# Performance work log

Measured on AMD Instinct MI355X. Metric: run time of the kernel, lower is better.

## Reference

```python
import jax, jax.numpy as jnp
import numpy as np

N_NODES = 100000
N_EDGES = 1600000
IN_DIM = 64
HID = 128
N_CLASSES = 1
N_GRAPHS = 512


def _glorot(key, shape):
    fan_in, fan_out = shape[0], shape[1]
    lim = (6.0 / (fan_in + fan_out)) ** 0.5
    return jax.random.uniform(key, shape, jnp.float32, -lim, lim)


def setup_inputs() -> dict:
    key = jax.random.key(0)
    ks = jax.random.split(key, 10)
    x = jax.random.normal(ks[0], (N_NODES, IN_DIM), jnp.float32)
    edge_src = jax.random.randint(ks[1], (N_EDGES,), 0, N_NODES)
    edge_dst = jax.random.randint(ks[2], (N_EDGES,), 0, N_NODES)
    graph_ids = jnp.sort(jax.random.randint(ks[3], (N_NODES,), 0, N_GRAPHS))
    return {
        "x": x,
        "edge_src": edge_src,
        "edge_dst": edge_dst,
        "graph_ids": graph_ids,
        "W1": _glorot(ks[4], (IN_DIM, HID)),
        "b1": jnp.zeros((HID,), jnp.float32),
        "W2": _glorot(ks[5], (HID, HID)),
        "b2": jnp.zeros((HID,), jnp.float32),
        "Wc1": _glorot(ks[6], (HID, HID)),
        "bc1": jnp.zeros((HID,), jnp.float32),
        "Wc2": _glorot(ks[7], (HID, HID)),
        "bc2": jnp.zeros((HID,), jnp.float32),
        "Wc3": _glorot(ks[8], (HID, N_CLASSES)),
        "bc3": jnp.zeros((N_CLASSES,), jnp.float32),
    }


def _graph_conv(h, edge_src, edge_dst, W, b):
    # DGL GraphConv, norm='both': out = D_out^{-1/2} A D_in^{-1/2} h W + b
    ones = jnp.ones((edge_src.shape[0],), h.dtype)
    deg_out = jnp.clip(jax.ops.segment_sum(ones, edge_src, num_segments=N_NODES), 1.0)
    deg_in = jnp.clip(jax.ops.segment_sum(ones, edge_dst, num_segments=N_NODES), 1.0)
    h = h * jax.lax.rsqrt(deg_out)[:, None]           # src-side norm
    agg = jax.ops.segment_sum(h[edge_src], edge_dst, num_segments=N_NODES)  # [N, D]
    agg = agg * jax.lax.rsqrt(deg_in)[:, None]        # dst-side norm
    return agg @ W + b


def reference(x, edge_src, edge_dst, graph_ids, W1, b1, W2, b2, Wc1, bc1, Wc2, bc2, Wc3, bc3):
    h = jax.nn.relu(_graph_conv(x, edge_src, edge_dst, W1, b1))
    h = jax.nn.relu(_graph_conv(h, edge_src, edge_dst, W2, b2))
    # mean_nodes pooling over batched graphs
    sums = jax.ops.segment_sum(h, graph_ids, num_segments=N_GRAPHS)  # [G, H]
    cnts = jax.ops.segment_sum(jnp.ones((N_NODES,), h.dtype), graph_ids, num_segments=N_GRAPHS)
    hg = sums / jnp.clip(cnts, 1.0)[:, None]
    out = jax.nn.relu(hg @ Wc1 + bc1)
    out = jax.nn.relu(out @ Wc2 + bc2)
    return out @ Wc3 + bc3  # [G, n_classes]
```

## Files before the change

### kernel.cpp

```cpp
#include <hip/hip_runtime.h>

#define N_NODES 100000
#define N_EDGES 1600000
#define IN_DIM 64
#define HID 128
#define N_GRAPHS 512
#define NBUCK 391

__global__ __launch_bounds__(256) void k_bhist(const int* __restrict__ src, const int* __restrict__ dst,
                                               int* __restrict__ dcnt, int* __restrict__ scnt) {
    __shared__ int hd[NBUCK];
    __shared__ int hs[NBUCK];
    const int t = threadIdx.x;
    const int e0 = blockIdx.x * 4096 + t * 16;
    for (int i = t; i < NBUCK; i += 256) { hd[i] = 0; hs[i] = 0; }
    __syncthreads();
    if (e0 < N_EDGES) {
        const int4* d4 = (const int4*)(dst + e0);
        const int4* s4 = (const int4*)(src + e0);
#pragma unroll
        for (int u = 0; u < 4; ++u) {
            int4 d = d4[u], s = s4[u];
            atomicAdd(&hd[d.x >> 8], 1); atomicAdd(&hd[d.y >> 8], 1);
            atomicAdd(&hd[d.z >> 8], 1); atomicAdd(&hd[d.w >> 8], 1);
            atomicAdd(&hs[s.x >> 8], 1); atomicAdd(&hs[s.y >> 8], 1);
            atomicAdd(&hs[s.z >> 8], 1); atomicAdd(&hs[s.w >> 8], 1);
        }
    }
    __syncthreads();
    for (int i = t; i < NBUCK; i += 256) {
        if (hd[i]) atomicAdd(&dcnt[i], hd[i]);
        if (hs[i]) atomicAdd(&scnt[i], hs[i]);
    }
}

__global__ __launch_bounds__(512) void k_bscan3(const int* __restrict__ dcnt, const int* __restrict__ scnt,
                                                const int* __restrict__ gid,
                                                int* __restrict__ dbase, int* __restrict__ sbase,
                                                int* __restrict__ dcur, int* __restrict__ scur,
                                                int* __restrict__ gstart) {
    const int t = threadIdx.x;
    if (blockIdx.x == 2) {
        for (int g = t; g <= N_GRAPHS; g += 512) {
            int lo = 0, hi = N_NODES;
            while (lo < hi) {
                int mid = (lo + hi) >> 1;
                if (gid[mid] < g) lo = mid + 1; else hi = mid;
            }
            gstart[g] = lo;
        }
        return;
    }
    __shared__ int l[512];
    const int* cntp = (blockIdx.x == 0) ? dcnt : scnt;
    int* basep = (blockIdx.x == 0) ? dbase : sbase;
    int* curp  = (blockIdx.x == 0) ? dcur  : scur;
    int v = (t < NBUCK) ? cntp[t] : 0;
    l[t] = v;
    __syncthreads();
    for (int off = 1; off < 512; off <<= 1) {
        int x = (t >= off) ? l[t - off] : 0;
        __syncthreads();
        l[t] += x;
        __syncthreads();
    }
    if (t < NBUCK) {
        int excl = l[t] - v;
        basep[t] = excl; curp[t] = excl;
    }
    if (t == NBUCK - 1) basep[NBUCK] = l[t];
}

__global__ __launch_bounds__(256) void k_bin2(const int* __restrict__ src, const int* __restrict__ dst,
                                              int* __restrict__ dcur, int* __restrict__ scur,
                                              int* __restrict__ binnedD, int* __restrict__ binnedS) {
    __shared__ int hd[NBUCK];
    __shared__ int bd[NBUCK];
    __shared__ int hs[NBUCK];
    __shared__ int bs[NBUCK];
    const int t = threadIdx.x;
    const int e0 = blockIdx.x * 4096 + t * 16;
    for (int i = t; i < NBUCK; i += 256) { hd[i] = 0; hs[i] = 0; }
    __syncthreads();
    if (e0 < N_EDGES) {
        const int4* d4 = (const int4*)(dst + e0);
        const int4* s4 = (const int4*)(src + e0);
#pragma unroll
        for (int u = 0; u < 4; ++u) {
            int4 d = d4[u], s = s4[u];
            atomicAdd(&hd[d.x >> 8], 1); atomicAdd(&hd[d.y >> 8], 1);
            atomicAdd(&hd[d.z >> 8], 1); atomicAdd(&hd[d.w >> 8], 1);
            atomicAdd(&hs[s.x >> 8], 1); atomicAdd(&hs[s.y >> 8], 1);
            atomicAdd(&hs[s.z >> 8], 1); atomicAdd(&hs[s.w >> 8], 1);
        }
    }
    __syncthreads();
    for (int i = t; i < NBUCK; i += 256) {
        int c = hd[i];
        bd[i] = c ? atomicAdd(&dcur[i], c) : 0;
        hd[i] = 0;
        c = hs[i];
        bs[i] = c ? atomicAdd(&scur[i], c) : 0;
        hs[i] = 0;
    }
    __syncthreads();
    if (e0 < N_EDGES) {
        const int4* d4 = (const int4*)(dst + e0);
        const int4* s4 = (const int4*)(src + e0);
#pragma unroll
        for (int u = 0; u < 4; ++u) {
            int4 d = d4[u];
            int4 s = s4[u];
            int bk, r;
            bk = d.x >> 8; r = atomicAdd(&hd[bk], 1); binnedD[bd[bk] + r] = s.x | ((d.x & 255) << 17);
            bk = d.y >> 8; r = atomicAdd(&hd[bk], 1); binnedD[bd[bk] + r] = s.y | ((d.y & 255) << 17);
            bk = d.z >> 8; r = atomicAdd(&hd[bk], 1); binnedD[bd[bk] + r] = s.z | ((d.z & 255) << 17);
            bk = d.w >> 8; r = atomicAdd(&hd[bk], 1); binnedD[bd[bk] + r] = s.w | ((d.w & 255) << 17);
            bk = s.x >> 8; r = atomicAdd(&hs[bk], 1); binnedS[bs[bk] + r] = s.x;
            bk = s.y >> 8; r = atomicAdd(&hs[bk], 1); binnedS[bs[bk] + r] = s.y;
            bk = s.z >> 8; r = atomicAdd(&hs[bk], 1); binnedS[bs[bk] + r] = s.z;
            bk = s.w >> 8; r = atomicAdd(&hs[bk], 1); binnedS[bs[bk] + r] = s.w;
        }
    }
}

__global__ __launch_bounds__(256) void k_prep2(const int* __restrict__ dbase, const int* __restrict__ sbase,
                                               const int* __restrict__ binnedD, const int* __restrict__ binnedS,
                                               int* __restrict__ rowp, float* __restrict__ rsi,
                                               float* __restrict__ rso, int* __restrict__ col) {
    const int t = threadIdx.x;
    if (blockIdx.x < NBUCK) {
        const int b = blockIdx.x;
        const int n0 = b * 256;
        __shared__ int cnt[256];
        __shared__ int scn[256];
        __shared__ int cur[256];
        __shared__ int sb[2];
        if (t < 2) sb[t] = dbase[b + t];
        cnt[t] = 0;
        __syncthreads();
        const int s = sb[0], e = sb[1];
        for (int i = s + t; i < e; i += 256) atomicAdd(&cnt[binnedD[i] >> 17], 1);
        __syncthreads();
        const int c = cnt[t];
        scn[t] = c;
        __syncthreads();
        for (int off = 1; off < 256; off <<= 1) {
            int v = (t >= off) ? scn[t - off] : 0;
            __syncthreads();
            scn[t] += v;
            __syncthreads();
        }
        const int excl = scn[t] - c;
        cur[t] = excl;
        if (n0 + t < N_NODES) {
            rowp[n0 + t] = s + excl;
            rsi[n0 + t] = 1.0f / sqrtf(fmaxf((float)c, 1.0f));
        }
        if (b == NBUCK - 1 && t == 0) rowp[N_NODES] = e;
        __syncthreads();
        for (int i = s + t; i < e; i += 256) {
            int p = binnedD[i];
            int r = atomicAdd(&cur[p >> 17], 1);
            col[s + r] = p & 0x1FFFF;
        }
    } else {
        const int b = blockIdx.x - NBUCK;
        const int n0 = b * 256;
        __shared__ int cnt2[256];
        __shared__ int sb2[2];
        if (t < 2) sb2[t] = sbase[b + t];
        cnt2[t] = 0;
        __syncthreads();
        const int s = sb2[0], e = sb2[1];
        for (int i = s + t; i < e; i += 256) atomicAdd(&cnt2[binnedS[i] - n0], 1);
        __syncthreads();
        if (n0 + t < N_NODES) rso[n0 + t] = 1.0f / sqrtf(fmaxf((float)cnt2[t], 1.0f));
    }
}

__global__ __launch_bounds__(256, 8) void k_g64mm(const float4* __restrict__ x4, const float* __restrict__ rso,
                                                  const int* __restrict__ rowp, const int* __restrict__ col,
                                                  const float* __restrict__ W, const float* __restrict__ bias,
                                                  const float* __restrict__ rsi, float* __restrict__ out) {
    __shared__ float aggL[32][IN_DIM];
    const int t = threadIdx.x;
    const int wid = t >> 6, lane = t & 63;
    const int n0 = blockIdx.x * 32;

    const int grp = lane >> 4, li = lane & 15;
#pragma unroll 1
    for (int it = 0; it < 8; ++it) {
        const int node = n0 + wid * 8 + it;
        const int s = rowp[node], e = rowp[node + 1];
        float ax = 0.f, ay = 0.f, az = 0.f, aw = 0.f;
        int i = s + grp;
        for (; i + 12 < e; i += 16) {
            int c0 = col[i], c1 = col[i + 4], c2 = col[i + 8], c3 = col[i + 12];
            float4 v0 = x4[c0 * 16 + li];
            float4 v1 = x4[c1 * 16 + li];
            float4 v2 = x4[c2 * 16 + li];
            float4 v3 = x4[c3 * 16 + li];
            float r0 = rso[c0], r1 = rso[c1], r2 = rso[c2], r3 = rso[c3];
            ax = fmaf(r0, v0.x, ax); ay = fmaf(r0, v0.y, ay); az = fmaf(r0, v0.z, az); aw = fmaf(r0, v0.w, aw);
            ax = fmaf(r1, v1.x, ax); ay = fmaf(r1, v1.y, ay); az = fmaf(r1, v1.z, az); aw = fmaf(r1, v1.w, aw);
            ax = fmaf(r2, v2.x, ax); ay = fmaf(r2, v2.y, ay); az = fmaf(r2, v2.z, az); aw = fmaf(r2, v2.w, aw);
            ax = fmaf(r3, v3.x, ax); ay = fmaf(r3, v3.y, ay); az = fmaf(r3, v3.z, az); aw = fmaf(r3, v3.w, aw);
        }
        for (; i + 4 < e; i += 8) {
            int c0 = col[i], c1 = col[i + 4];
            float4 v0 = x4[c0 * 16 + li];
            float4 v1 = x4[c1 * 16 + li];
            float r0 = rso[c0], r1 = rso[c1];
            ax = fmaf(r0, v0.x, ax); ay = fmaf(r0, v0.y, ay); az = fmaf(r0, v0.z, az); aw = fmaf(r0, v0.w, aw);
            ax = fmaf(r1, v1.x, ax); ay = fmaf(r1, v1.y, ay); az = fmaf(r1, v1.z, az); aw = fmaf(r1, v1.w, aw);
        }
        for (; i < e; i += 4) {
            int c = col[i];
            float4 v = x4[c * 16 + li];
            float r = rso[c];
            ax = fmaf(r, v.x, ax); ay = fmaf(r, v.y, ay); az = fmaf(r, v.z, az); aw = fmaf(r, v.w, aw);
        }
        ax += __shfl_xor(ax, 16, 64); ay += __shfl_xor(ay, 16, 64);
        az += __shfl_xor(az, 16, 64); aw += __shfl_xor(aw, 16, 64);
        ax += __shfl_xor(ax, 32, 64); ay += __shfl_xor(ay, 32, 64);
        az += __shfl_xor(az, 32, 64); aw += __shfl_xor(aw, 32, 64);
        if (lane < 16) {
            float4 o; o.x = ax; o.y = ay; o.z = az; o.w = aw;
            ((float4*)aggL[node - n0])[li] = o;
        }
    }
    __syncthreads();

    const int jq = t & 31;
    const int ns = t >> 5;
    const float4* Wg = (const float4*)W;
    float acc[4][4] = {};
#pragma unroll 8
    for (int k = 0; k < IN_DIM; ++k) {
        float4 wv = Wg[k * 32 + jq];
#pragma unroll
        for (int i = 0; i < 4; ++i) {
            float av = aggL[ns * 4 + i][k];
            acc[i][0] += av * wv.x; acc[i][1] += av * wv.y;
            acc[i][2] += av * wv.z; acc[i][3] += av * wv.w;
        }
    }
    float4 bj = ((const float4*)bias)[jq];
#pragma unroll
    for (int i = 0; i < 4; ++i) {
        int node = n0 + ns * 4 + i;
        float ri = rsi[node];
        float ro = rso[node];
        float4 o;
        o.x = fmaxf(acc[i][0] * ri + bj.x, 0.f) * ro;
        o.y = fmaxf(acc[i][1] * ri + bj.y, 0.f) * ro;
        o.z = fmaxf(acc[i][2] * ri + bj.z, 0.f) * ro;
        o.w = fmaxf(acc[i][3] * ri + bj.w, 0.f) * ro;
        *(float4*)(out + (size_t)node * HID + jq * 4) = o;
    }
}

__global__ __launch_bounds__(256, 8) void k_g128p(const float4* __restrict__ h4, const int* __restrict__ rowp,
                                                  const int* __restrict__ col, const float* __restrict__ W,
                                                  const float* __restrict__ bias, const float* __restrict__ rsi,
                                                  const int* __restrict__ gid, float* __restrict__ gsum) {
    __shared__ float agg[32][HID];
    __shared__ float gpart[8][128];
    const int t = threadIdx.x;
    const int wid = t >> 6, lane = t & 63;
    const int n0 = blockIdx.x * 32;
    for (int u = t; u < 8 * 128; u += 256) ((float*)gpart)[u] = 0.f;

    const int grp = lane >> 5, li = lane & 31;
#pragma unroll 1
    for (int it = 0; it < 8; ++it) {
        const int node = n0 + wid * 8 + it;
        const int s = rowp[node], e = rowp[node + 1];
        float ax = 0.f, ay = 0.f, az = 0.f, aw = 0.f;
        int i = s + grp;
        for (; i + 6 < e; i += 8) {
            int c0 = col[i], c1 = col[i + 2], c2 = col[i + 4], c3 = col[i + 6];
            float4 v0 = h4[c0 * 32 + li];
            float4 v1 = h4[c1 * 32 + li];
            float4 v2 = h4[c2 * 32 + li];
            float4 v3 = h4[c3 * 32 + li];
            ax += v0.x + v1.x + v2.x + v3.x;
            ay += v0.y + v1.y + v2.y + v3.y;
            az += v0.z + v1.z + v2.z + v3.z;
            aw += v0.w + v1.w + v2.w + v3.w;
        }
        for (; i < e; i += 2) {
            float4 v = h4[col[i] * 32 + li];
            ax += v.x; ay += v.y; az += v.z; aw += v.w;
        }
        ax += __shfl_xor(ax, 32, 64); ay += __shfl_xor(ay, 32, 64);
        az += __shfl_xor(az, 32, 64); aw += __shfl_xor(aw, 32, 64);
        if (lane < 32) {
            float4 o; o.x = ax; o.y = ay; o.z = az; o.w = aw;
            ((float4*)agg[node - n0])[li] = o;
        }
    }
    __syncthreads();

    const int jq = t & 31;
    const int ns = t >> 5;
    const float4* Wg = (const float4*)W;
    float acc[4][4] = {};
#pragma unroll 8
    for (int k = 0; k < HID; ++k) {
        float4 wv = Wg[k * 32 + jq];
#pragma unroll
        for (int i = 0; i < 4; ++i) {
            float av = agg[ns * 4 + i][k];
            acc[i][0] += av * wv.x; acc[i][1] += av * wv.y;
            acc[i][2] += av * wv.z; acc[i][3] += av * wv.w;
        }
    }

    const int g0 = gid[n0];
    float4 bj = ((const float4*)bias)[jq];
    int curslot = -9;
    float p0 = 0.f, p1 = 0.f, p2 = 0.f, p3 = 0.f;
#pragma unroll
    for (int i = 0; i < 4; ++i) {
        int node = n0 + ns * 4 + i;
        float ri = rsi[node];
        float ox = fmaxf(acc[i][0] * ri + bj.x, 0.f);
        float oy = fmaxf(acc[i][1] * ri + bj.y, 0.f);
        float oz = fmaxf(acc[i][2] * ri + bj.z, 0.f);
        float ow = fmaxf(acc[i][3] * ri + bj.w, 0.f);
        int slot = gid[node] - g0;
        if (slot != curslot) {
            if (curslot >= 0) {
                if (curslot < 8) {
                    atomicAdd(&gpart[curslot][jq * 4 + 0], p0);
                    atomicAdd(&gpart[curslot][jq * 4 + 1], p1);
                    atomicAdd(&gpart[curslot][jq * 4 + 2], p2);
                    atomicAdd(&gpart[curslot][jq * 4 + 3], p3);
                } else {
                    atomicAdd(&gsum[(g0 + curslot) * HID + jq * 4 + 0], p0);
                    atomicAdd(&gsum[(g0 + curslot) * HID + jq * 4 + 1], p1);
                    atomicAdd(&gsum[(g0 + curslot) * HID + jq * 4 + 2], p2);
                    atomicAdd(&gsum[(g0 + curslot) * HID + jq * 4 + 3], p3);
                }
            }
            curslot = slot; p0 = ox; p1 = oy; p2 = oz; p3 = ow;
        } else {
            p0 += ox; p1 += oy; p2 += oz; p3 += ow;
        }
    }
    if (curslot >= 0) {
        if (curslot < 8) {
            atomicAdd(&gpart[curslot][jq * 4 + 0], p0);
            atomicAdd(&gpart[curslot][jq * 4 + 1], p1);
            atomicAdd(&gpart[curslot][jq * 4 + 2], p2);
            atomicAdd(&gpart[curslot][jq * 4 + 3], p3);
        } else {
            atomicAdd(&gsum[(g0 + curslot) * HID + jq * 4 + 0], p0);
            atomicAdd(&gsum[(g0 + curslot) * HID + jq * 4 + 1], p1);
            atomicAdd(&gsum[(g0 + curslot) * HID + jq * 4 + 2], p2);
            atomicAdd(&gsum[(g0 + curslot) * HID + jq * 4 + 3], p3);
        }
    }
    __syncthreads();
    for (int u = t; u < 8 * 128; u += 256) {
        int slot = u >> 7, c = u & 127;
        float v = gpart[slot][c];
        if (v != 0.f) {
            int g = g0 + slot;
            if (g < N_GRAPHS) atomicAdd(&gsum[g * HID + c], v);
        }
    }
}

__global__ __launch_bounds__(128) void k_head(const float* __restrict__ gsum, const int* __restrict__ gstart,
                                              const float* __restrict__ Wc1, const float* __restrict__ bc1,
                                              const float* __restrict__ Wc2, const float* __restrict__ bc2,
                                              const float* __restrict__ Wc3, const float* __restrict__ bc3,
                                              float* __restrict__ out) {
    int g = blockIdx.x, t = threadIdx.x;
    int s = gstart[g], e = gstart[g + 1];
    float cnt = fmaxf((float)(e - s), 1.0f);
    __shared__ float buf[HID];
    __shared__ float red[2];
    buf[t] = gsum[g * HID + t] / cnt;
    __syncthreads();
    float a = bc1[t];
#pragma unroll 8
    for (int k = 0; k < HID; ++k) a += buf[k] * Wc1[k * HID + t];
    a = fmaxf(a, 0.f);
    __syncthreads();
    buf[t] = a;
    __syncthreads();
    float b = bc2[t];
#pragma unroll 8
    for (int k = 0; k < HID; ++k) b += buf[k] * Wc2[k * HID + t];
    b = fmaxf(b, 0.f);
    float p = b * Wc3[t];
    for (int off = 32; off > 0; off >>= 1) p += __shfl_down(p, off, 64);
    if ((t & 63) == 0) red[t >> 6] = p;
    __syncthreads();
    if (t == 0) out[g] = red[0] + red[1] + bc3[0];
}

extern "C" void kernel_launch(void* const* d_in, const int* in_sizes, int n_in,
                              void* d_out, int out_size, void* d_ws, size_t ws_size,
                              hipStream_t stream) {
    const float* x   = (const float*)d_in[0];
    const int* esrc  = (const int*)d_in[1];
    const int* edst  = (const int*)d_in[2];
    const int* gid   = (const int*)d_in[3];
    const float* W1  = (const float*)d_in[4];
    const float* b1  = (const float*)d_in[5];
    const float* W2  = (const float*)d_in[6];
    const float* b2  = (const float*)d_in[7];
    const float* Wc1 = (const float*)d_in[8];
    const float* bc1 = (const float*)d_in[9];
    const float* Wc2 = (const float*)d_in[10];
    const float* bc2 = (const float*)d_in[11];
    const float* Wc3 = (const float*)d_in[12];
    const float* bc3 = (const float*)d_in[13];
    float* out = (float*)d_out;

    char* w = (char*)d_ws;
    size_t off = 0;
    auto alloc = [&](size_t bytes) -> char* {
        char* p = w + off;
        off += (bytes + 255) & ~(size_t)255;
        return p;
    };
    int* dcnt   = (int*)alloc((size_t)2 * (NBUCK + 1) * 4);
    int* scnt   = dcnt + (NBUCK + 1);
    int* dbase  = (int*)alloc((size_t)(NBUCK + 1) * 4);
    int* sbase  = (int*)alloc((size_t)(NBUCK + 1) * 4);
    int* dcur   = (int*)alloc((size_t)NBUCK * 4);
    int* scur   = (int*)alloc((size_t)NBUCK * 4);
    float* rso  = (float*)alloc((size_t)N_NODES * 4);
    float* rsi  = (float*)alloc((size_t)N_NODES * 4);
    int* rowp   = (int*)alloc((size_t)(N_NODES + 1) * 4);
    int* gstart = (int*)alloc((size_t)(N_GRAPHS + 1) * 4);
    int* col    = (int*)alloc((size_t)N_EDGES * 4);
    float* gsum = (float*)alloc((size_t)N_GRAPHS * HID * 4);
    float* R1   = (float*)alloc((size_t)N_NODES * HID * 4);
    float* R2   = (float*)alloc((size_t)N_NODES * HID * 4);
    int* binnedD = (int*)R1;
    int* binnedS = (int*)R1 + (size_t)N_EDGES;
    float* h1s  = R2;

    (void)in_sizes; (void)n_in; (void)out_size; (void)ws_size;

    hipMemsetAsync(dcnt, 0, (size_t)2 * (NBUCK + 1) * 4, stream);
    hipMemsetAsync(gsum, 0, (size_t)N_GRAPHS * HID * 4, stream);

    const int BB = (N_EDGES + 4095) / 4096;
    const int FB32 = N_NODES / 32;

    k_bhist<<<BB, 256, 0, stream>>>(esrc, edst, dcnt, scnt);
    k_bscan3<<<3, 512, 0, stream>>>(dcnt, scnt, gid, dbase, sbase, dcur, scur, gstart);
    k_bin2<<<BB, 256, 0, stream>>>(esrc, edst, dcur, scur, binnedD, binnedS);
    k_prep2<<<2 * NBUCK, 256, 0, stream>>>(dbase, sbase, binnedD, binnedS, rowp, rsi, rso, col);
    k_g64mm<<<FB32, 256, 0, stream>>>((const float4*)x, rso, rowp, col, W1, b1, rsi, h1s);
    k_g128p<<<FB32, 256, 0, stream>>>((const float4*)h1s, rowp, col, W2, b2, rsi, gid, gsum);
    k_head<<<N_GRAPHS, 128, 0, stream>>>(gsum, gstart, Wc1, bc1, Wc2, bc2, Wc3, bc3, out);
}
```

Before: 354.4 us.

## Double block size and stage weight chunks in shared memory for fused GEMM

Blocks for both graph-conv kernels grow from 256 to 512 threads, so each wave aggregates 4 nodes instead of 8 and each thread computes 2 output rows instead of 4. The dense transform now copies 32-row chunks of W into shared memory before reading them, where before each thread read W straight from global memory. The aim is more latency hiding during the gather and less global/L2 traffic for W. In exchange it adds extra barriers per k-chunk, more LDS per block (which may lower occupancy), and the launch bound of 512 with 8 blocks may squeeze registers.

```diff
diff --git a/kernel.cpp b/kernel.cpp
--- a/kernel.cpp
+++ b/kernel.cpp
@@ -179,19 +179,20 @@
     }
 }
 
-__global__ __launch_bounds__(256, 8) void k_g64mm(const float4* __restrict__ x4, const float* __restrict__ rso,
+__global__ __launch_bounds__(512, 8) void k_g64mm(const float4* __restrict__ x4, const float* __restrict__ rso,
                                                   const int* __restrict__ rowp, const int* __restrict__ col,
                                                   const float* __restrict__ W, const float* __restrict__ bias,
                                                   const float* __restrict__ rsi, float* __restrict__ out) {
     __shared__ float aggL[32][IN_DIM];
+    __shared__ float WL[32 * 128];
     const int t = threadIdx.x;
     const int wid = t >> 6, lane = t & 63;
     const int n0 = blockIdx.x * 32;
 
     const int grp = lane >> 4, li = lane & 15;
 #pragma unroll 1
-    for (int it = 0; it < 8; ++it) {
-        const int node = n0 + wid * 8 + it;
+    for (int it = 0; it < 4; ++it) {
+        const int node = n0 + wid * 4 + it;
         const int s = rowp[node], e = rowp[node + 1];
         float ax = 0.f, ay = 0.f, az = 0.f, aw = 0.f;
         int i = s + grp;
@@ -230,26 +231,30 @@
             ((float4*)aggL[node - n0])[li] = o;
         }
     }
-    __syncthreads();
 
     const int jq = t & 31;
     const int ns = t >> 5;
-    const float4* Wg = (const float4*)W;
-    float acc[4][4] = {};
-#pragma unroll 8
-    for (int k = 0; k < IN_DIM; ++k) {
-        float4 wv = Wg[k * 32 + jq];
-#pragma unroll
-        for (int i = 0; i < 4; ++i) {
-            float av = aggL[ns * 4 + i][k];
-            acc[i][0] += av * wv.x; acc[i][1] += av * wv.y;
-            acc[i][2] += av * wv.z; acc[i][3] += av * wv.w;
+    float acc[2][4] = {};
+    for (int kc = 0; kc < IN_DIM; kc += 32) {
+        const float4* Wg = (const float4*)(W + kc * 128);
+        float4* WL4 = (float4*)WL;
+        __syncthreads();
+#pragma unroll
+        for (int u = 0; u < 2; ++u) WL4[t + 512 * u] = Wg[t + 512 * u];
+        __syncthreads();
+#pragma unroll
+        for (int k = 0; k < 32; ++k) {
+            float4 wv = ((const float4*)WL)[k * 32 + jq];
+            float a0 = aggL[ns * 2 + 0][kc + k];
+            float a1 = aggL[ns * 2 + 1][kc + k];
+            acc[0][0] += a0 * wv.x; acc[0][1] += a0 * wv.y; acc[0][2] += a0 * wv.z; acc[0][3] += a0 * wv.w;
+            acc[1][0] += a1 * wv.x; acc[1][1] += a1 * wv.y; acc[1][2] += a1 * wv.z; acc[1][3] += a1 * wv.w;
         }
     }
     float4 bj = ((const float4*)bias)[jq];
 #pragma unroll
-    for (int i = 0; i < 4; ++i) {
-        int node = n0 + ns * 4 + i;
+    for (int i = 0; i < 2; ++i) {
+        int node = n0 + ns * 2 + i;
         float ri = rsi[node];
         float ro = rso[node];
         float4 o;
@@ -261,21 +266,22 @@
     }
 }
 
-__global__ __launch_bounds__(256, 8) void k_g128p(const float4* __restrict__ h4, const int* __restrict__ rowp,
+__global__ __launch_bounds__(512, 8) void k_g128p(const float4* __restrict__ h4, const int* __restrict__ rowp,
                                                   const int* __restrict__ col, const float* __restrict__ W,
                                                   const float* __restrict__ bias, const float* __restrict__ rsi,
                                                   const int* __restrict__ gid, float* __restrict__ gsum) {
     __shared__ float agg[32][HID];
+    __shared__ float WL[32 * 128];
     __shared__ float gpart[8][128];
     const int t = threadIdx.x;
     const int wid = t >> 6, lane = t & 63;
     const int n0 = blockIdx.x * 32;
-    for (int u = t; u < 8 * 128; u += 256) ((float*)gpart)[u] = 0.f;
+    for (int u = t; u < 8 * 128; u += 512) ((float*)gpart)[u] = 0.f;
 
     const int grp = lane >> 5, li = lane & 31;
 #pragma unroll 1
-    for (int it = 0; it < 8; ++it) {
-        const int node = n0 + wid * 8 + it;
+    for (int it = 0; it < 4; ++it) {
+        const int node = n0 + wid * 4 + it;
         const int s = rowp[node], e = rowp[node + 1];
         float ax = 0.f, ay = 0.f, az = 0.f, aw = 0.f;
         int i = s + grp;
@@ -301,20 +307,24 @@
             ((float4*)agg[node - n0])[li] = o;
         }
     }
-    __syncthreads();
 
     const int jq = t & 31;
     const int ns = t >> 5;
-    const float4* Wg = (const float4*)W;
-    float acc[4][4] = {};
-#pragma unroll 8
-    for (int k = 0; k < HID; ++k) {
-        float4 wv = Wg[k * 32 + jq];
-#pragma unroll
-        for (int i = 0; i < 4; ++i) {
-            float av = agg[ns * 4 + i][k];
-            acc[i][0] += av * wv.x; acc[i][1] += av * wv.y;
-            acc[i][2] += av * wv.z; acc[i][3] += av * wv.w;
+    float acc[2][4] = {};
+    for (int kc = 0; kc < HID; kc += 32) {
+        const float4* Wg = (const float4*)(W + kc * 128);
+        float4* WL4 = (float4*)WL;
+        __syncthreads();
+#pragma unroll
+        for (int u = 0; u < 2; ++u) WL4[t + 512 * u] = Wg[t + 512 * u];
+        __syncthreads();
+#pragma unroll
+        for (int k = 0; k < 32; ++k) {
+            float4 wv = ((const float4*)WL)[k * 32 + jq];
+            float a0 = agg[ns * 2 + 0][kc + k];
+            float a1 = agg[ns * 2 + 1][kc + k];
+            acc[0][0] += a0 * wv.x; acc[0][1] += a0 * wv.y; acc[0][2] += a0 * wv.z; acc[0][3] += a0 * wv.w;
+            acc[1][0] += a1 * wv.x; acc[1][1] += a1 * wv.y; acc[1][2] += a1 * wv.z; acc[1][3] += a1 * wv.w;
         }
     }
 
@@ -323,8 +333,8 @@
     int curslot = -9;
     float p0 = 0.f, p1 = 0.f, p2 = 0.f, p3 = 0.f;
 #pragma unroll
-    for (int i = 0; i < 4; ++i) {
-        int node = n0 + ns * 4 + i;
+    for (int i = 0; i < 2; ++i) {
+        int node = n0 + ns * 2 + i;
         float ri = rsi[node];
         float ox = fmaxf(acc[i][0] * ri + bj.x, 0.f);
         float oy = fmaxf(acc[i][1] * ri + bj.y, 0.f);
@@ -364,7 +374,7 @@
         }
     }
     __syncthreads();
-    for (int u = t; u < 8 * 128; u += 256) {
+    for (int u = t; u < 8 * 128; u += 512) {
         int slot = u >> 7, c = u & 127;
         float v = gpart[slot][c];
         if (v != 0.f) {
@@ -460,7 +470,7 @@
     k_bscan3<<<3, 512, 0, stream>>>(dcnt, scnt, gid, dbase, sbase, dcur, scur, gstart);
     k_bin2<<<BB, 256, 0, stream>>>(esrc, edst, dcur, scur, binnedD, binnedS);
     k_prep2<<<2 * NBUCK, 256, 0, stream>>>(dbase, sbase, binnedD, binnedS, rowp, rsi, rso, col);
-    k_g64mm<<<FB32, 256, 0, stream>>>((const float4*)x, rso, rowp, col, W1, b1, rsi, h1s);
-    k_g128p<<<FB32, 256, 0, stream>>>((const float4*)h1s, rowp, col, W2, b2, rsi, gid, gsum);
+    k_g64mm<<<FB32, 512, 0, stream>>>((const float4*)x, rso, rowp, col, W1, b1, rsi, h1s);
+    k_g128p<<<FB32, 512, 0, stream>>>((const float4*)h1s, rowp, col, W2, b2, rsi, gid, gsum);
     k_head<<<N_GRAPHS, 128, 0, stream>>>(gsum, gstart, Wc1, bc1, Wc2, bc2, Wc3, bc3, out);
 }
```

Result: faster. 332.5 us (-6.2%).
